# Performance work log

Hardware: AMD Instinct MI355X
Metric: run time of the kernel (lower is better)

## Reference

```python
import jax, jax.numpy as jnp
import numpy as np

D_EMBED = 1024
NUM_HEADS = 16
D_HEAD = D_EMBED // NUM_HEADS


def setup_inputs() -> dict:
    key = jax.random.key(0)
    ks = jax.random.split(key, 7)
    B, S = 2, 2048
    s = 1.0 / np.sqrt(D_EMBED)
    return {
        "hidden_states": jax.random.normal(ks[0], (B, S, D_EMBED), dtype=jnp.float32),
        "Wq": jax.random.uniform(ks[1], (D_EMBED, D_EMBED), jnp.float32, -s, s),
        "bq": jax.random.uniform(ks[2], (D_EMBED,), jnp.float32, -s, s),
        "Wk": jax.random.uniform(ks[3], (D_EMBED, D_EMBED), jnp.float32, -s, s),
        "bk": jax.random.uniform(ks[4], (D_EMBED,), jnp.float32, -s, s),
        "Wv": jax.random.uniform(ks[5], (D_EMBED, D_EMBED), jnp.float32, -s, s),
        "bv": jax.random.uniform(ks[6], (D_EMBED,), jnp.float32, -s, s),
    }


def _heads(x):
    # [B,S,D] -> [B,H,S,dh]
    B, S, _ = x.shape
    return x.reshape(B, S, NUM_HEADS, D_HEAD).transpose(0, 2, 1, 3)


def reference(hidden_states, Wq, bq, Wk, bk, Wv, bv):
    # torch Linear: y = x @ W.T + b
    q = _heads(jnp.einsum("bsd,ed->bse", hidden_states, Wq) + bq)
    k = _heads(jnp.einsum("bsd,ed->bse", hidden_states, Wk) + bk)
    v = _heads(jnp.einsum("bsd,ed->bse", hidden_states, Wv) + bv)
    scores = jnp.einsum("bhqd,bhkd->bhqk", q, k) / jnp.sqrt(jnp.float32(D_HEAD))
    probs = jax.nn.softmax(scores, axis=-1)  # dropout: eval mode (identity)
    ctx = jnp.einsum("bhqk,bhkd->bhqd", probs, v)  # [B,H,S,dh]
    B, H, S, dh = ctx.shape
    ctx = ctx.transpose(0, 2, 1, 3).reshape(B, S, H * dh)
    return ctx, probs
```

## Files before the change

### kernel.cpp

```cpp
#include <hip/hip_runtime.h>
#include <cmath>

#define SEQ 2048
#define NH  16

using bf16x8 = __attribute__((ext_vector_type(8))) short;
using f32x4  = __attribute__((ext_vector_type(4))) float;
using u16x8  = __attribute__((ext_vector_type(8))) unsigned short;
using u16x4  = __attribute__((ext_vector_type(4))) unsigned short;

#define MFMA __builtin_amdgcn_mfma_f32_16x16x32_bf16

static __device__ __forceinline__ unsigned short f2b(float f) {
  unsigned int x = __float_as_uint(f);
  x += 0x7fffu + ((x >> 16) & 1u);
  return (unsigned short)(x >> 16);
}

static __device__ __forceinline__ u16x8 cvt8(f32x4 a, f32x4 b) {
  u16x8 o;
  o[0] = f2b(a[0]); o[1] = f2b(a[1]); o[2] = f2b(a[2]); o[3] = f2b(a[3]);
  o[4] = f2b(b[0]); o[5] = f2b(b[1]); o[6] = f2b(b[2]); o[7] = f2b(b[3]);
  return o;
}

__global__ __launch_bounds__(256) void convert_kernel(
    const float* __restrict__ x, const float* __restrict__ wq,
    const float* __restrict__ wk, const float* __restrict__ wv,
    unsigned short* __restrict__ dst) {
  int bid = blockIdx.x;
  const float* src;
  size_t off;
  if (bid < 2048)      { src = x;  off = (size_t)bid * 2048; }
  else if (bid < 2560) { src = wq; off = (size_t)(bid - 2048) * 2048; dst += 4194304; }
  else if (bid < 3072) { src = wk; off = (size_t)(bid - 2560) * 2048; dst += 4194304 + 1048576; }
  else                 { src = wv; off = (size_t)(bid - 3072) * 2048; dst += 4194304 + 2097152; }
  size_t i = off + (size_t)threadIdx.x * 8;
  f32x4 a = *(const f32x4*)(src + i);
  f32x4 b = *(const f32x4*)(src + i + 4);
  *(u16x8*)(dst + i) = cvt8(a, b);
}

template <int VAR>
__global__ __launch_bounds__(256) void gemm_qkv(
    const unsigned short* __restrict__ x_bf,
    const unsigned short* __restrict__ w_bf,
    const float* __restrict__ bq, const float* __restrict__ bk,
    const float* __restrict__ bv,
    unsigned short* __restrict__ q_ws, unsigned short* __restrict__ k_ws,
    unsigned short* __restrict__ vt_ws) {
  const int st  = blockIdx.x;
  const int et  = blockIdx.y;
  const int tid = threadIdx.x;
  const int w = tid >> 6, l = tid & 63, c = l & 15, g = l >> 4;
  const int wr = w >> 1, wc = w & 1;

  __shared__ unsigned short Xt[128 * 32];
  __shared__ unsigned short Wt[128 * 32];

  const int wrow_base = (VAR == 0 ? et * 128 : 2048 + et * 128);

  f32x4 acc[4][4];
#pragma unroll
  for (int m = 0; m < 4; ++m)
#pragma unroll
    for (int n = 0; n < 4; ++n) acc[m][n] = f32x4{0.f, 0.f, 0.f, 0.f};

  for (int kb = 0; kb < 32; ++kb) {
    __syncthreads();
#pragma unroll
    for (int i = 0; i < 2; ++i) {
      int row   = i * 64 + w * 16 + (l >> 2);
      int chunk = (l & 3) ^ ((row >> 1) & 3);
      const unsigned short* gx = x_bf + (size_t)(st * 128 + row) * 1024 + kb * 32 + chunk * 8;
      const unsigned short* gw = w_bf + (size_t)(wrow_base + row) * 1024 + kb * 32 + chunk * 8;
      __builtin_amdgcn_global_load_lds(
          (const __attribute__((address_space(1))) void*)gx,
          (__attribute__((address_space(3))) void*)&Xt[(i * 64 + w * 16) * 32], 16, 0, 0);
      __builtin_amdgcn_global_load_lds(
          (const __attribute__((address_space(1))) void*)gw,
          (__attribute__((address_space(3))) void*)&Wt[(i * 64 + w * 16) * 32], 16, 0, 0);
    }
    asm volatile("s_waitcnt vmcnt(0)" ::: "memory");
    __syncthreads();

    bf16x8 af[4], bfr[4];
#pragma unroll
    for (int m = 0; m < 4; ++m) {
      int ar = wr * 64 + m * 16 + c;
      int br = wc * 64 + m * 16 + c;
      int ach = g ^ ((ar >> 1) & 3);
      int bch = g ^ ((br >> 1) & 3);
      if (VAR == 0) {
        af[m]  = *(const bf16x8*)(&Wt[ar * 32 + ach * 8]);
        bfr[m] = *(const bf16x8*)(&Xt[br * 32 + bch * 8]);
      } else {
        af[m]  = *(const bf16x8*)(&Xt[ar * 32 + ach * 8]);
        bfr[m] = *(const bf16x8*)(&Wt[br * 32 + bch * 8]);
      }
    }
#pragma unroll
    for (int m = 0; m < 4; ++m)
#pragma unroll
      for (int n = 0; n < 4; ++n)
        acc[m][n] = MFMA(af[m], bfr[n], acc[m][n], 0, 0, 0);
  }

  const float QSC = 0.125f * 1.44269504088896340736f;
  if (VAR == 0) {
    const bool isq = (et < 8);
#pragma unroll
    for (int m = 0; m < 4; ++m) {
      int e0 = et * 128 + wr * 64 + m * 16 + g * 4;
      int eh = e0 & 1023;
      int h = eh >> 6, d0 = eh & 63;
#pragma unroll
      for (int n = 0; n < 4; ++n) {
        int s = st * 128 + wc * 64 + n * 16 + c;
        int b = s >> 11, sl = s & 2047;
        u16x4 p;
        if (isq) {
#pragma unroll
          for (int r = 0; r < 4; ++r) p[r] = f2b((acc[m][n][r] + bq[eh + r]) * QSC);
          *(u16x4*)(&q_ws[((size_t)(b * NH + h) * SEQ + sl) * 64 + d0]) = p;
        } else {
#pragma unroll
          for (int r = 0; r < 4; ++r) p[r] = f2b(acc[m][n][r] + bk[eh + r]);
          *(u16x4*)(&k_ws[((size_t)(b * NH + h) * SEQ + sl) * 64 + d0]) = p;
        }
      }
    }
  } else {
#pragma unroll
    for (int m = 0; m < 4; ++m) {
      int s0 = st * 128 + wr * 64 + m * 16 + g * 4;
      int b = s0 >> 11, sl0 = s0 & 2047;
#pragma unroll
      for (int n = 0; n < 4; ++n) {
        int e = et * 128 + wc * 64 + n * 16 + c;
        int h = e >> 6, d = e & 63;
        float bias = bv[e];
        u16x4 p;
#pragma unroll
        for (int r = 0; r < 4; ++r) p[r] = f2b(acc[m][n][r] + bias);
        *(u16x4*)(&vt_ws[((size_t)(b * NH + h) * 64 + d) * SEQ + sl0]) = p;
      }
    }
  }
}

static __device__ __forceinline__ void stage_tile(
    unsigned short* dstLds, const unsigned short* src_base, int src_stride_u16, int tid) {
#pragma unroll
  for (int i = 0; i < 2; ++i) {
    int flat = (i * 256 + tid) * 16;
    int row  = flat >> 7;
    int colb = flat & 127;
    const unsigned short* src = src_base + (size_t)row * src_stride_u16 + (colb >> 1);
    int dst = row * 64 + ((colb ^ ((row & 7) << 4)) >> 1);
    *(u16x8*)(&dstLds[dst]) = *(const u16x8*)src;
  }
}

__global__ __launch_bounds__(256) void attn_kernel(
    const unsigned short* __restrict__ q_ws, const unsigned short* __restrict__ k_ws,
    const unsigned short* __restrict__ vt_ws, float* __restrict__ out) {
  const int qt  = blockIdx.x;
  const int bh  = blockIdx.y;
  const int tid = threadIdx.x;
  const int w = tid >> 6, l = tid & 63, c = l & 15, g = l >> 4;

  __shared__ unsigned short Kl[64 * 64];
  __shared__ unsigned short Vt[64 * 64];
  __shared__ unsigned short Pl[4][16 * 64];

  const int qrow = qt * 64 + w * 16 + c;
  const unsigned short* qp = q_ws + ((size_t)bh * SEQ + qrow) * 64;
  bf16x8 qf[2];
  qf[0] = *(const bf16x8*)(qp + g * 8);
  qf[1] = *(const bf16x8*)(qp + 32 + g * 8);

  float mrun = -INFINITY, lsum = 0.f;

  for (int kt = 0; kt < 32; ++kt) {
    __syncthreads();
    stage_tile(Kl, k_ws + ((size_t)bh * SEQ + kt * 64) * 64, 64, tid);
    __syncthreads();
    f32x4 sa[4];
#pragma unroll
    for (int m4 = 0; m4 < 4; ++m4) sa[m4] = f32x4{0.f,0.f,0.f,0.f};
#pragma unroll
    for (int ks = 0; ks < 2; ++ks)
#pragma unroll
      for (int m4 = 0; m4 < 4; ++m4) {
        int row = m4 * 16 + c;
        bf16x8 kf = *(const bf16x8*)(&Kl[row * 64 + ((ks * 32 + g * 8) ^ ((row & 7) << 3))]);
        sa[m4] = MFMA(kf, qf[ks], sa[m4], 0, 0, 0);
      }
    float tmax = sa[0][0];
#pragma unroll
    for (int m4 = 0; m4 < 4; ++m4)
#pragma unroll
      for (int r = 0; r < 4; ++r) tmax = fmaxf(tmax, sa[m4][r]);
    tmax = fmaxf(tmax, __shfl_xor(tmax, 16));
    tmax = fmaxf(tmax, __shfl_xor(tmax, 32));
    float mn   = fmaxf(mrun, tmax);
    float corr = exp2f(mrun - mn);
    float ts = 0.f;
#pragma unroll
    for (int m4 = 0; m4 < 4; ++m4)
#pragma unroll
      for (int r = 0; r < 4; ++r) ts += exp2f(sa[m4][r] - mn);
    ts += __shfl_xor(ts, 16);
    ts += __shfl_xor(ts, 32);
    lsum = lsum * corr + ts;
    mrun = mn;
  }
  const float invl = 1.f / lsum;

  f32x4 ctx[4];
#pragma unroll
  for (int f = 0; f < 4; ++f) ctx[f] = f32x4{0.f,0.f,0.f,0.f};

  float* probs_row = out + (size_t)2 * SEQ * 1024 + ((size_t)bh * SEQ + qrow) * SEQ;

  for (int kt = 0; kt < 32; ++kt) {
    __syncthreads();
    stage_tile(Kl, k_ws + ((size_t)bh * SEQ + kt * 64) * 64, 64, tid);
    stage_tile(Vt, vt_ws + (size_t)bh * 64 * SEQ + kt * 64, SEQ, tid);
    __syncthreads();
    f32x4 sa[4];
#pragma unroll
    for (int m4 = 0; m4 < 4; ++m4) sa[m4] = f32x4{0.f,0.f,0.f,0.f};
#pragma unroll
    for (int ks = 0; ks < 2; ++ks)
#pragma unroll
      for (int m4 = 0; m4 < 4; ++m4) {
        int row = m4 * 16 + c;
        bf16x8 kf = *(const bf16x8*)(&Kl[row * 64 + ((ks * 32 + g * 8) ^ ((row & 7) << 3))]);
        sa[m4] = MFMA(kf, qf[ks], sa[m4], 0, 0, 0);
      }
#pragma unroll
    for (int m4 = 0; m4 < 4; ++m4) {
      f32x4 pv;
#pragma unroll
      for (int r = 0; r < 4; ++r) pv[r] = exp2f(sa[m4][r] - mrun) * invl;
      *(f32x4*)(probs_row + kt * 64 + m4 * 16 + g * 4) = pv;
      u16x4 pb;
#pragma unroll
      for (int r = 0; r < 4; ++r) pb[r] = f2b(pv[r]);
      *(u16x4*)(&Pl[w][c * 64 + ((m4 * 16 + g * 4) ^ ((c & 7) << 3))]) = pb;
    }
#pragma unroll
    for (int ks = 0; ks < 2; ++ks) {
      bf16x8 pa = *(const bf16x8*)(&Pl[w][c * 64 + ((ks * 32 + g * 8) ^ ((c & 7) << 3))]);
#pragma unroll
      for (int f = 0; f < 4; ++f) {
        int row = f * 16 + c;
        bf16x8 vb = *(const bf16x8*)(&Vt[row * 64 + ((ks * 32 + g * 8) ^ ((row & 7) << 3))]);
        ctx[f] = MFMA(pa, vb, ctx[f], 0, 0, 0);
      }
    }
  }

  const int b = bh >> 4, h = bh & 15;
#pragma unroll
  for (int f = 0; f < 4; ++f)
#pragma unroll
    for (int r = 0; r < 4; ++r) {
      int s = qt * 64 + w * 16 + g * 4 + r;
      out[((size_t)b * SEQ + s) * 1024 + h * 64 + f * 16 + c] = ctx[f][r];
    }
}

extern "C" void kernel_launch(void* const* d_in, const int* in_sizes, int n_in,
                              void* d_out, int out_size, void* d_ws, size_t ws_size,
                              hipStream_t stream) {
  (void)in_sizes; (void)n_in; (void)out_size; (void)ws_size;
  const float* x  = (const float*)d_in[0];
  const float* wq = (const float*)d_in[1];
  const float* bq = (const float*)d_in[2];
  const float* wk = (const float*)d_in[3];
  const float* bk = (const float*)d_in[4];
  const float* wv = (const float*)d_in[5];
  const float* bv = (const float*)d_in[6];

  unsigned short* xw_bf = (unsigned short*)d_ws;
  unsigned short* x_bf  = xw_bf;
  unsigned short* w_bf  = xw_bf + 4194304;
  unsigned short* q_ws  = xw_bf + 7340032;
  unsigned short* k_ws  = q_ws + 4194304;
  unsigned short* vt_ws = k_ws + 4194304;
  float* out = (float*)d_out;

  convert_kernel<<<3584, 256, 0, stream>>>(x, wq, wk, wv, xw_bf);
  gemm_qkv<0><<<dim3(32, 16), 256, 0, stream>>>(x_bf, w_bf, bq, bk, bv, q_ws, k_ws, vt_ws);
  gemm_qkv<1><<<dim3(32, 8), 256, 0, stream>>>(x_bf, w_bf, bq, bk, bv, q_ws, k_ws, vt_ws);
  attn_kernel<<<dim3(32, 32), 256, 0, stream>>>(q_ws, k_ws, vt_ws, out);
}
```

Baseline: 263.0 us.

## Single-pass attention without max subtraction, buffering bf16 probs in LDS

Replaces the two-pass online-softmax attention with a single pass. Each block handles 16 query rows, and each wave computes scores for a 16-key slice read straight from global memory instead of through staged LDS tiles. The unnormalised exp values are kept as bf16 in a 64KB LDS buffer and fed to the PV MFMA. Normalisation is applied at the end, and fp32 probs are written out from that buffer. This removes the duplicate QK^T pass and the max tracking. In exchange it drops max subtraction, so it could overflow on large scores, writes probs rounded to bf16, and the large LDS footprint limits occupancy.

```diff
diff --git a/kernel.cpp b/kernel.cpp
--- a/kernel.cpp
+++ b/kernel.cpp
@@ -15,6 +15,10 @@
   unsigned int x = __float_as_uint(f);
   x += 0x7fffu + ((x >> 16) & 1u);
   return (unsigned short)(x >> 16);
+}
+
+static __device__ __forceinline__ float b2f(unsigned short u) {
+  return __uint_as_float(((unsigned int)u) << 16);
 }
 
 static __device__ __forceinline__ u16x8 cvt8(f32x4 a, f32x4 b) {
@@ -149,19 +153,6 @@
   }
 }
 
-static __device__ __forceinline__ void stage_tile(
-    unsigned short* dstLds, const unsigned short* src_base, int src_stride_u16, int tid) {
-#pragma unroll
-  for (int i = 0; i < 2; ++i) {
-    int flat = (i * 256 + tid) * 16;
-    int row  = flat >> 7;
-    int colb = flat & 127;
-    const unsigned short* src = src_base + (size_t)row * src_stride_u16 + (colb >> 1);
-    int dst = row * 64 + ((colb ^ ((row & 7) << 4)) >> 1);
-    *(u16x8*)(&dstLds[dst]) = *(const u16x8*)src;
-  }
-}
-
 __global__ __launch_bounds__(256) void attn_kernel(
     const unsigned short* __restrict__ q_ws, const unsigned short* __restrict__ k_ws,
     const unsigned short* __restrict__ vt_ws, float* __restrict__ out) {
@@ -170,107 +161,79 @@
   const int tid = threadIdx.x;
   const int w = tid >> 6, l = tid & 63, c = l & 15, g = l >> 4;
 
-  __shared__ unsigned short Kl[64 * 64];
-  __shared__ unsigned short Vt[64 * 64];
-  __shared__ unsigned short Pl[4][16 * 64];
-
-  const int qrow = qt * 64 + w * 16 + c;
-  const unsigned short* qp = q_ws + ((size_t)bh * SEQ + qrow) * 64;
-  bf16x8 qf[2];
-  qf[0] = *(const bf16x8*)(qp + g * 8);
-  qf[1] = *(const bf16x8*)(qp + 32 + g * 8);
-
-  float mrun = -INFINITY, lsum = 0.f;
+  __shared__ unsigned short Pl[16 * 2048];
+  __shared__ float Ls[4][16];
+  __shared__ float invL[16];
+
+  const unsigned short* qp = q_ws + ((size_t)bh * SEQ + qt * 16 + c) * 64 + g * 8;
+  bf16x8 qf0 = *(const bf16x8*)(qp);
+  bf16x8 qf1 = *(const bf16x8*)(qp + 32);
+
+  const unsigned short* kp  = k_ws  + ((size_t)bh * SEQ + w * 16 + c) * 64 + g * 8;
+  const unsigned short* vp  = vt_ws + ((size_t)bh * 64 + w * 16 + c) * SEQ + g * 8;
+
+  float lsum = 0.f;
+  f32x4 ctx = f32x4{0.f, 0.f, 0.f, 0.f};
+  const int swz = (c & 7) << 3;
 
   for (int kt = 0; kt < 32; ++kt) {
-    __syncthreads();
-    stage_tile(Kl, k_ws + ((size_t)bh * SEQ + kt * 64) * 64, 64, tid);
-    __syncthreads();
-    f32x4 sa[4];
-#pragma unroll
-    for (int m4 = 0; m4 < 4; ++m4) sa[m4] = f32x4{0.f,0.f,0.f,0.f};
-#pragma unroll
-    for (int ks = 0; ks < 2; ++ks)
-#pragma unroll
-      for (int m4 = 0; m4 < 4; ++m4) {
-        int row = m4 * 16 + c;
-        bf16x8 kf = *(const bf16x8*)(&Kl[row * 64 + ((ks * 32 + g * 8) ^ ((row & 7) << 3))]);
-        sa[m4] = MFMA(kf, qf[ks], sa[m4], 0, 0, 0);
-      }
-    float tmax = sa[0][0];
-#pragma unroll
-    for (int m4 = 0; m4 < 4; ++m4)
-#pragma unroll
-      for (int r = 0; r < 4; ++r) tmax = fmaxf(tmax, sa[m4][r]);
-    tmax = fmaxf(tmax, __shfl_xor(tmax, 16));
-    tmax = fmaxf(tmax, __shfl_xor(tmax, 32));
-    float mn   = fmaxf(mrun, tmax);
-    float corr = exp2f(mrun - mn);
-    float ts = 0.f;
-#pragma unroll
-    for (int m4 = 0; m4 < 4; ++m4)
-#pragma unroll
-      for (int r = 0; r < 4; ++r) ts += exp2f(sa[m4][r] - mn);
+    bf16x8 kf0 = *(const bf16x8*)(kp + (size_t)kt * 64 * 64);
+    bf16x8 kf1 = *(const bf16x8*)(kp + (size_t)kt * 64 * 64 + 32);
+    f32x4 sa = f32x4{0.f, 0.f, 0.f, 0.f};
+    sa = MFMA(kf0, qf0, sa, 0, 0, 0);
+    sa = MFMA(kf1, qf1, sa, 0, 0, 0);
+
+    f32x4 p;
+#pragma unroll
+    for (int r = 0; r < 4; ++r) p[r] = exp2f(sa[r]);
+    float ts = p[0] + p[1] + p[2] + p[3];
     ts += __shfl_xor(ts, 16);
     ts += __shfl_xor(ts, 32);
-    lsum = lsum * corr + ts;
-    mrun = mn;
-  }
-  const float invl = 1.f / lsum;
-
-  f32x4 ctx[4];
-#pragma unroll
-  for (int f = 0; f < 4; ++f) ctx[f] = f32x4{0.f,0.f,0.f,0.f};
-
-  float* probs_row = out + (size_t)2 * SEQ * 1024 + ((size_t)bh * SEQ + qrow) * SEQ;
-
-  for (int kt = 0; kt < 32; ++kt) {
+    lsum += ts;
+
+    u16x4 pb;
+#pragma unroll
+    for (int r = 0; r < 4; ++r) pb[r] = f2b(p[r]);
+    *(u16x4*)(&Pl[c * 2048 + ((kt * 64 + w * 16 + g * 4) ^ swz)]) = pb;
+
     __syncthreads();
-    stage_tile(Kl, k_ws + ((size_t)bh * SEQ + kt * 64) * 64, 64, tid);
-    stage_tile(Vt, vt_ws + (size_t)bh * 64 * SEQ + kt * 64, SEQ, tid);
-    __syncthreads();
-    f32x4 sa[4];
-#pragma unroll
-    for (int m4 = 0; m4 < 4; ++m4) sa[m4] = f32x4{0.f,0.f,0.f,0.f};
-#pragma unroll
-    for (int ks = 0; ks < 2; ++ks)
-#pragma unroll
-      for (int m4 = 0; m4 < 4; ++m4) {
-        int row = m4 * 16 + c;
-        bf16x8 kf = *(const bf16x8*)(&Kl[row * 64 + ((ks * 32 + g * 8) ^ ((row & 7) << 3))]);
-        sa[m4] = MFMA(kf, qf[ks], sa[m4], 0, 0, 0);
-      }
-#pragma unroll
-    for (int m4 = 0; m4 < 4; ++m4) {
+
+#pragma unroll
+    for (int ks = 0; ks < 2; ++ks) {
+      bf16x8 pa = *(const bf16x8*)(&Pl[c * 2048 + ((kt * 64 + ks * 32 + g * 8) ^ swz)]);
+      bf16x8 vb = *(const bf16x8*)(vp + (size_t)kt * 64 + ks * 32);
+      ctx = MFMA(pa, vb, ctx, 0, 0, 0);
+    }
+  }
+
+  if (g == 0) Ls[w][c] = lsum;
+  __syncthreads();
+  if (tid < 16) invL[tid] = 1.f / (Ls[0][tid] + Ls[1][tid] + Ls[2][tid] + Ls[3][tid]);
+  __syncthreads();
+
+  const int b = bh >> 4, h = bh & 15;
+#pragma unroll
+  for (int r = 0; r < 4; ++r) {
+    int s = qt * 16 + g * 4 + r;
+    out[((size_t)b * SEQ + s) * 1024 + h * 64 + w * 16 + c] = ctx[r] * invL[g * 4 + r];
+  }
+
+  {
+    const int row = tid >> 4, lane16 = tid & 15;
+    const float il = invL[row];
+    const int rswz = (row & 7) << 3;
+    float* pr = out + (size_t)2 * SEQ * 1024 +
+                ((size_t)bh * SEQ + qt * 16 + row) * SEQ;
+#pragma unroll
+    for (int i = 0; i < 32; ++i) {
+      int col = (i * 16 + lane16) * 4;
+      u16x4 pb = *(const u16x4*)(&Pl[row * 2048 + (col ^ rswz)]);
       f32x4 pv;
 #pragma unroll
-      for (int r = 0; r < 4; ++r) pv[r] = exp2f(sa[m4][r] - mrun) * invl;
-      *(f32x4*)(probs_row + kt * 64 + m4 * 16 + g * 4) = pv;
-      u16x4 pb;
-#pragma unroll
-      for (int r = 0; r < 4; ++r) pb[r] = f2b(pv[r]);
-      *(u16x4*)(&Pl[w][c * 64 + ((m4 * 16 + g * 4) ^ ((c & 7) << 3))]) = pb;
-    }
-#pragma unroll
-    for (int ks = 0; ks < 2; ++ks) {
-      bf16x8 pa = *(const bf16x8*)(&Pl[w][c * 64 + ((ks * 32 + g * 8) ^ ((c & 7) << 3))]);
-#pragma unroll
-      for (int f = 0; f < 4; ++f) {
-        int row = f * 16 + c;
-        bf16x8 vb = *(const bf16x8*)(&Vt[row * 64 + ((ks * 32 + g * 8) ^ ((row & 7) << 3))]);
-        ctx[f] = MFMA(pa, vb, ctx[f], 0, 0, 0);
-      }
-    }
-  }
-
-  const int b = bh >> 4, h = bh & 15;
-#pragma unroll
-  for (int f = 0; f < 4; ++f)
-#pragma unroll
-    for (int r = 0; r < 4; ++r) {
-      int s = qt * 64 + w * 16 + g * 4 + r;
-      out[((size_t)b * SEQ + s) * 1024 + h * 64 + f * 16 + c] = ctx[f][r];
-    }
+      for (int r = 0; r < 4; ++r) pv[r] = b2f(pb[r]) * il;
+      *(f32x4*)(pr + col) = pv;
+    }
+  }
 }
 
 extern "C" void kernel_launch(void* const* d_in, const int* in_sizes, int n_in,
@@ -296,5 +259,5 @@
   convert_kernel<<<3584, 256, 0, stream>>>(x, wq, wk, wv, xw_bf);
   gemm_qkv<0><<<dim3(32, 16), 256, 0, stream>>>(x_bf, w_bf, bq, bk, bv, q_ws, k_ws, vt_ws);
   gemm_qkv<1><<<dim3(32, 8), 256, 0, stream>>>(x_bf, w_bf, bq, bk, bv, q_ws, k_ws, vt_ws);
-  attn_kernel<<<dim3(32, 32), 256, 0, stream>>>(q_ws, k_ws, vt_ws, out);
-}
+  attn_kernel<<<dim3(128, 32), 256, 0, stream>>>(q_ws, k_ws, vt_ws, out);
+}
```

Measured after the change: 402.6 us. 53.1% more time.
